# Performance work log

Hardware: AMD Instinct MI355X
Metric: run time of the kernel (lower is better)

## Reference

```python
import jax, jax.numpy as jnp
import numpy as np

B, C_IN, C_OUT = 16, 256, 128
V_RAW, N_VERT, K = 10242, 40962, 7


def setup_inputs() -> dict:
    key = jax.random.key(0)
    k1, k2, k3, k4, k5, k6 = jax.random.split(key, 6)
    x = jax.random.normal(k1, (B, C_IN, V_RAW), dtype=jnp.float32)
    W = jax.random.normal(k2, (C_OUT, C_IN), dtype=jnp.float32) * (1.0 / np.sqrt(C_IN))
    b = jax.random.normal(k3, (C_OUT,), dtype=jnp.float32) * 0.01
    up_neigh_indices = jax.random.randint(k4, (N_VERT, K), 0, N_VERT, dtype=jnp.int64)
    down_indices = jax.random.randint(k5, (V_RAW,), 0, N_VERT, dtype=jnp.int64)
    max_pool_indices = jax.random.randint(k6, (B, C_OUT, V_RAW), 0, K, dtype=jnp.int64)
    return {"x": x, "W": W, "b": b,
            "up_neigh_indices": up_neigh_indices,
            "down_indices": down_indices,
            "max_pool_indices": max_pool_indices}


def _feats_indices(n_feats: int, n_raw_vertices: int) -> np.ndarray:
    # torch: floor(linspace(0, n_feats, num=n_raw_vertices*n_feats)); last -= 1
    fi = np.floor(np.linspace(0.0, float(n_feats), num=n_raw_vertices * n_feats))
    fi[-1] -= 1
    return fi.astype(np.int64)


def reference(x, W, b, up_neigh_indices, down_indices, max_pool_indices):
    n_samples, in_feats, n_raw = x.shape
    n_vertices = up_neigh_indices.shape[0]
    out_feats = W.shape[0]

    # per-vertex linear projection: (B, Cin, V) -> (B, Cout, V)
    h = jnp.einsum('bcv,oc->bov', x, W) + b[None, :, None]

    # neighbor table at coarse vertices: (V_raw, K)
    neigh = up_neigh_indices[down_indices]

    # vertices_indices[b, f, v] = neigh[v, max_pool_indices[b, f, v]]
    vi = neigh[jnp.arange(n_raw)[None, None, :], max_pool_indices]  # (B, Cout, V_raw)

    # flatten exactly like torch (row-major over (Cout, V_raw))
    h_flat = h.reshape(n_samples, out_feats * n_raw)
    vi_flat = vi.reshape(n_samples, out_feats * n_raw)
    fi = jnp.asarray(_feats_indices(out_feats, n_raw))  # (Cout*V_raw,) static

    y = jnp.zeros((n_samples, out_feats, n_vertices), dtype=h.dtype)
    y = y.at[jnp.arange(n_samples)[:, None], fi[None, :], vi_flat].set(h_flat)
    return y
```

## Files before the change

kernel.cpp:

```cpp
#include <hip/hip_runtime.h>

#define NB    16
#define CIN   256
#define COUT  128
#define VRAW  10242
#define NVERT 40962
#define QSZ   10241
#define NROW  (NB * COUT)

typedef __attribute__((ext_vector_type(8))) short short8;
typedef __attribute__((ext_vector_type(4))) float floatx4;
typedef float f4u __attribute__((ext_vector_type(4), aligned(4)));

__device__ inline unsigned short f2bf(float f) {
    unsigned u = __builtin_bit_cast(unsigned, f);
    u += 0x7fffu + ((u >> 16) & 1u);
    return (unsigned short)(u >> 16);
}

__global__ __launch_bounds__(256) void convw_kernel(const float* __restrict__ W,
                                                    unsigned short* __restrict__ Wbf) {
    int i = blockIdx.x * 256 + threadIdx.x;
    Wbf[i] = f2bf(W[i]);
}

__global__ __launch_bounds__(256) void prep_kernel(const int* __restrict__ up,
                                                   const int* __restrict__ down,
                                                   unsigned short* __restrict__ T16) {
    int idx = blockIdx.x * 256 + threadIdx.x;
    if (idx >= VRAW * 8) return;
    int v = idx >> 3;
    int k = idx & 7;
    if (k > 6) k = 6;
    T16[idx] = (unsigned short)up[down[v] * 7 + k];
}

__global__ __launch_bounds__(256) void tgt_kernel(const int* __restrict__ mpi,
                                                  const unsigned short* __restrict__ T16,
                                                  unsigned* __restrict__ tgt32) {
    const int r  = blockIdx.y;
    const int vp = blockIdx.x * 256 + threadIdx.x;
    if (vp >= VRAW / 2) return;
    const int2 kk = *(const int2*)(mpi + (size_t)r * VRAW + 2 * (size_t)vp);
    const unsigned t0 = T16[(2 * vp)     * 8 + kk.x];
    const unsigned t1 = T16[(2 * vp + 1) * 8 + kk.y];
    tgt32[(size_t)r * (VRAW / 2) + vp] = t0 | (t1 << 16);
}

#define KC 64
#define VT 128
__global__ __launch_bounds__(256) void gemm_kernel(const float* __restrict__ x,
                                                   const unsigned short* __restrict__ Wbf,
                                                   const float* __restrict__ bias,
                                                   float* __restrict__ h) {
    __shared__ unsigned short xt[VT * KC];
    const int b    = blockIdx.y;
    const int v0   = blockIdx.x * VT;
    const int tid  = threadIdx.x;
    const int wv   = tid >> 6;
    const int lane = tid & 63;
    const int mn   = lane & 15;
    const int q    = lane >> 4;
    const int ow   = (wv & 1) * 64;
    const int vwl  = (wv >> 1) * 64;

    floatx4 acc[4][4];
#pragma unroll
    for (int ot = 0; ot < 4; ot++)
#pragma unroll
        for (int vt = 0; vt < 4; vt++) acc[ot][vt] = (floatx4)0.f;

    for (int c0 = 0; c0 < CIN; c0 += KC) {
#pragma unroll
        for (int i = 0; i < 2; i++) {
            const int tile  = tid + i * 256;
            const int cg    = tile >> 5;
            const int vg    = tile & 31;
            const int vglob = v0 + vg * 4;
            const float* xp = x + ((size_t)b * CIN + c0 + cg * 4) * VRAW + vglob;
            float vals[4][4];
            if (vglob + 3 < VRAW) {
#pragma unroll
                for (int cc = 0; cc < 4; cc++) {
                    f4u rv = *(const f4u*)(xp + (size_t)cc * VRAW);
                    vals[cc][0] = rv.x; vals[cc][1] = rv.y;
                    vals[cc][2] = rv.z; vals[cc][3] = rv.w;
                }
            } else {
#pragma unroll
                for (int cc = 0; cc < 4; cc++)
#pragma unroll
                    for (int jj = 0; jj < 4; jj++)
                        vals[cc][jj] = (vglob + jj < VRAW) ? xp[(size_t)cc * VRAW + jj] : 0.f;
            }
            const int swbase = (cg ^ ((vg & 7) << 1)) << 2;
#pragma unroll
            for (int jj = 0; jj < 4; jj++) {
                const int vloc = vg * 4 + jj;
                unsigned long long pk =
                      (unsigned long long)f2bf(vals[0][jj])
                    | ((unsigned long long)f2bf(vals[1][jj]) << 16)
                    | ((unsigned long long)f2bf(vals[2][jj]) << 32)
                    | ((unsigned long long)f2bf(vals[3][jj]) << 48);
                *(unsigned long long*)&xt[vloc * KC + swbase] = pk;
            }
        }
        __syncthreads();

#pragma unroll
        for (int kk = 0; kk < 2; kk++) {
            short8 bfrag[4];
#pragma unroll
            for (int vt = 0; vt < 4; vt++) {
                const int vloc = vwl + vt * 16 + mn;
                const int cqb  = kk * 8 + q * 2;
                const int cq   = cqb ^ (((vloc >> 2) & 7) << 1);
                bfrag[vt] = *(const short8*)&xt[vloc * KC + (cq << 2)];
            }
#pragma unroll
            for (int ot = 0; ot < 4; ot++) {
                const short8 afrag = *(const short8*)(Wbf + (size_t)(ow + ot * 16 + mn) * CIN
                                                      + c0 + kk * 32 + q * 8);
#pragma unroll
                for (int vt = 0; vt < 4; vt++)
                    acc[ot][vt] = __builtin_amdgcn_mfma_f32_16x16x32_bf16(afrag, bfrag[vt], acc[ot][vt], 0, 0, 0);
            }
        }
        __syncthreads();
    }

#pragma unroll
    for (int ot = 0; ot < 4; ot++) {
#pragma unroll
        for (int r = 0; r < 4; r++) {
            const int o  = ow + ot * 16 + q * 4 + r;
            const float bi = bias[o];
#pragma unroll
            for (int vt = 0; vt < 4; vt++) {
                const int v = v0 + vwl + vt * 16 + mn;
                if (v < VRAW) h[((size_t)b * COUT + o) * VRAW + v] = acc[ot][vt][r] + bi;
            }
        }
    }
}

template<int USE_TGT>
__global__ __launch_bounds__(512, 6) void scatter_kernel(const unsigned* __restrict__ tgt32,
                                                         const unsigned short* __restrict__ T16,
                                                         const int* __restrict__ mpi,
                                                         const float* __restrict__ h,
                                                         float* __restrict__ y) {
    __shared__ __align__(16) unsigned st[QSZ];
    const int bid = blockIdx.x;
    const int x8  = bid & 7;
    const int j   = bid >> 3;
    const int r   = x8 * 256 + (j >> 2);
    const int qi  = j & 3;
    const int tbase = qi * QSZ;
    const int qlen  = min(QSZ, NVERT - tbase);
    const int tid   = threadIdx.x;

    uint4* st4 = (uint4*)st;
    const uint4 z4 = make_uint4(0u, 0u, 0u, 0u);
#pragma unroll
    for (int i = 0; i < 5; i++) st4[tid + i * 512] = z4;
    if (tid == 0) st[10240] = 0u;
    __syncthreads();

    if (USE_TGT) {
        const unsigned* tRow = tgt32 + (size_t)r * (VRAW / 2);
#pragma unroll
        for (int it = 0; it < 10; it++) {
            const int vp = tid + it * 512;
            const unsigned tw = tRow[vp];
            const unsigned lt0 = (tw & 0xffffu) - (unsigned)tbase;
            const unsigned lt1 = (tw >> 16)     - (unsigned)tbase;
            if (lt0 < (unsigned)qlen) atomicMax(&st[lt0], (unsigned)(2 * vp + 1));
            if (lt1 < (unsigned)qlen) atomicMax(&st[lt1], (unsigned)(2 * vp + 2));
        }
        if (tid == 0) {
            const unsigned tw = tRow[5120];
            const unsigned lt0 = (tw & 0xffffu) - (unsigned)tbase;
            const unsigned lt1 = (tw >> 16)     - (unsigned)tbase;
            if (lt0 < (unsigned)qlen) atomicMax(&st[lt0], 10241u);
            if (lt1 < (unsigned)qlen) atomicMax(&st[lt1], 10242u);
        }
    } else {
        const int* mpiRow = mpi + (size_t)r * VRAW;
#pragma unroll 4
        for (int it = 0; it < 20; it++) {
            const int v = tid + it * 512;
            const int k = mpiRow[v];
            const uint4 tt = *(const uint4*)(T16 + (size_t)v * 8);
            const unsigned w0 = (k & 2) ? tt.y : tt.x;
            const unsigned w1 = (k & 2) ? tt.w : tt.z;
            const unsigned wsel = (k & 4) ? w1 : w0;
            const unsigned t = (wsel >> ((k & 1) * 16)) & 0xffffu;
            const unsigned lt = t - (unsigned)tbase;
            if (lt < (unsigned)qlen) atomicMax(&st[lt], (unsigned)(v + 1));
        }
        if (tid < 2) {
            const int v = 10240 + tid;
            const int k = mpiRow[v];
            const uint4 tt = *(const uint4*)(T16 + (size_t)v * 8);
            const unsigned w0 = (k & 2) ? tt.y : tt.x;
            const unsigned w1 = (k & 2) ? tt.w : tt.z;
            const unsigned wsel = (k & 4) ? w1 : w0;
            const unsigned t = (wsel >> ((k & 1) * 16)) & 0xffffu;
            const unsigned lt = t - (unsigned)tbase;
            if (lt < (unsigned)qlen) atomicMax(&st[lt], (unsigned)(v + 1));
        }
    }
    __syncthreads();

    const float* hRow = h + (size_t)r * VRAW;
    float* yRow = y + (size_t)r * NVERT + tbase;
#pragma unroll
    for (int i2 = 0; i2 < 4; i2++) {
        const int i = tid + i2 * 512;
        const uint4 s4 = st4[i];
        f4u out;
        out.x = s4.x ? hRow[s4.x - 1u] : 0.f;
        out.y = s4.y ? hRow[s4.y - 1u] : 0.f;
        out.z = s4.z ? hRow[s4.z - 1u] : 0.f;
        out.w = s4.w ? hRow[s4.w - 1u] : 0.f;
        *(f4u*)(yRow + 4 * i) = out;
    }
    {
        const int i = tid + 2048;
        if (4 * i + 3 < qlen) {
            const uint4 s4 = st4[i];
            f4u out;
            out.x = s4.x ? hRow[s4.x - 1u] : 0.f;
            out.y = s4.y ? hRow[s4.y - 1u] : 0.f;
            out.z = s4.z ? hRow[s4.z - 1u] : 0.f;
            out.w = s4.w ? hRow[s4.w - 1u] : 0.f;
            *(f4u*)(yRow + 4 * i) = out;
        }
    }
    const int base = qlen & ~3;
    if (tid < qlen - base) {
        const int lt = base + tid;
        const unsigned s = st[lt];
        yRow[lt] = s ? hRow[s - 1u] : 0.f;
    }
}

extern "C" void kernel_launch(void* const* d_in, const int* in_sizes, int n_in,
                              void* d_out, int out_size, void* d_ws, size_t ws_size,
                              hipStream_t stream) {
    const float* x    = (const float*)d_in[0];
    const float* W    = (const float*)d_in[1];
    const float* bias = (const float*)d_in[2];
    const int*   up   = (const int*)d_in[3];
    const int*   down = (const int*)d_in[4];
    const int*   mpi  = (const int*)d_in[5];
    float* y = (float*)d_out;

    const size_t off_h   = 65536;
    const size_t off_t16 = off_h + (size_t)NROW * VRAW * 4;
    const size_t off_tgt = off_t16 + (size_t)VRAW * 8 * 2;
    const size_t need    = off_tgt + (size_t)NROW * (VRAW / 2) * 4;

    unsigned short* Wbf = (unsigned short*)d_ws;
    float* h            = (float*)((char*)d_ws + off_h);
    unsigned short* T16 = (unsigned short*)((char*)d_ws + off_t16);
    unsigned* tgt32     = (unsigned*)((char*)d_ws + off_tgt);
    const bool use_tgt  = ws_size >= need;

    convw_kernel<<<COUT * CIN / 256, 256, 0, stream>>>(W, Wbf);
    prep_kernel<<<(VRAW * 8 + 255) / 256, 256, 0, stream>>>(up, down, T16);
    if (use_tgt) {
        dim3 tgrid((VRAW / 2 + 255) / 256, NROW);
        tgt_kernel<<<tgrid, 256, 0, stream>>>(mpi, T16, tgt32);
    }

    dim3 ggrid((VRAW + VT - 1) / VT, NB);
    gemm_kernel<<<ggrid, 256, 0, stream>>>(x, Wbf, bias, h);

    if (use_tgt)
        scatter_kernel<1><<<NROW * 4, 512, 0, stream>>>(tgt32, T16, mpi, h, y);
    else
        scatter_kernel<0><<<NROW * 4, 512, 0, stream>>>(tgt32, T16, mpi, h, y);
}
```

Baseline: 690.7 us.

## Double-buffer GEMM input tile in LDS with register prefetch of next K chunk

The GEMM kernel now keeps two LDS buffers for the bf16 x tile. It issues the global loads for the next 64-channel chunk into registers before running the MFMAs on the current chunk, then converts and writes them into the other buffer afterwards. This removes one barrier per iteration and is meant to hide global load latency behind matrix math. In exchange it doubles LDS use (32KB) and holds the 32 prefetched floats per thread in registers, which may lower occupancy.

```diff
diff --git a/kernel.cpp b/kernel.cpp
--- a/kernel.cpp
+++ b/kernel.cpp
@@ -49,11 +49,12 @@
 
 #define KC 64
 #define VT 128
+
 __global__ __launch_bounds__(256) void gemm_kernel(const float* __restrict__ x,
                                                    const unsigned short* __restrict__ Wbf,
                                                    const float* __restrict__ bias,
                                                    float* __restrict__ h) {
-    __shared__ unsigned short xt[VT * KC];
+    __shared__ unsigned short xt[2][VT * KC];
     const int b    = blockIdx.y;
     const int v0   = blockIdx.x * VT;
     const int tid  = threadIdx.x;
@@ -70,43 +71,62 @@
 #pragma unroll
         for (int vt = 0; vt < 4; vt++) acc[ot][vt] = (floatx4)0.f;
 
-    for (int c0 = 0; c0 < CIN; c0 += KC) {
-#pragma unroll
-        for (int i = 0; i < 2; i++) {
-            const int tile  = tid + i * 256;
-            const int cg    = tile >> 5;
-            const int vg    = tile & 31;
-            const int vglob = v0 + vg * 4;
-            const float* xp = x + ((size_t)b * CIN + c0 + cg * 4) * VRAW + vglob;
-            float vals[4][4];
-            if (vglob + 3 < VRAW) {
-#pragma unroll
-                for (int cc = 0; cc < 4; cc++) {
-                    f4u rv = *(const f4u*)(xp + (size_t)cc * VRAW);
-                    vals[cc][0] = rv.x; vals[cc][1] = rv.y;
-                    vals[cc][2] = rv.z; vals[cc][3] = rv.w;
-                }
-            } else {
-#pragma unroll
-                for (int cc = 0; cc < 4; cc++)
-#pragma unroll
-                    for (int jj = 0; jj < 4; jj++)
-                        vals[cc][jj] = (vglob + jj < VRAW) ? xp[(size_t)cc * VRAW + jj] : 0.f;
-            }
-            const int swbase = (cg ^ ((vg & 7) << 1)) << 2;
-#pragma unroll
-            for (int jj = 0; jj < 4; jj++) {
-                const int vloc = vg * 4 + jj;
-                unsigned long long pk =
-                      (unsigned long long)f2bf(vals[0][jj])
-                    | ((unsigned long long)f2bf(vals[1][jj]) << 16)
-                    | ((unsigned long long)f2bf(vals[2][jj]) << 32)
-                    | ((unsigned long long)f2bf(vals[3][jj]) << 48);
-                *(unsigned long long*)&xt[vloc * KC + swbase] = pk;
-            }
-        }
+    float vals[2][4][4];
+
+#define LOADX(c0_)                                                                  \
+    {                                                                               \
+        _Pragma("unroll")                                                           \
+        for (int i = 0; i < 2; i++) {                                               \
+            const int cg    = (tid >> 5) + i * 8;                                   \
+            const int vg    = tid & 31;                                             \
+            const int vglob = v0 + vg * 4;                                          \
+            const float* xp = x + ((size_t)b * CIN + (c0_) + cg * 4) * VRAW + vglob;\
+            if (vglob + 3 < VRAW) {                                                 \
+                _Pragma("unroll")                                                   \
+                for (int cc = 0; cc < 4; cc++) {                                    \
+                    f4u rv = *(const f4u*)(xp + (size_t)cc * VRAW);                 \
+                    vals[i][cc][0] = rv.x; vals[i][cc][1] = rv.y;                   \
+                    vals[i][cc][2] = rv.z; vals[i][cc][3] = rv.w;                   \
+                }                                                                   \
+            } else {                                                                \
+                _Pragma("unroll")                                                   \
+                for (int cc = 0; cc < 4; cc++)                                      \
+                    _Pragma("unroll")                                               \
+                    for (int jj = 0; jj < 4; jj++)                                  \
+                        vals[i][cc][jj] = (vglob + jj < VRAW) ? xp[(size_t)cc * VRAW + jj] : 0.f; \
+            }                                                                       \
+        }                                                                           \
+    }
+
+#define CWRITE(buf_)                                                                \
+    {                                                                               \
+        _Pragma("unroll")                                                           \
+        for (int i = 0; i < 2; i++) {                                               \
+            const int cg     = (tid >> 5) + i * 8;                                  \
+            const int vg     = tid & 31;                                            \
+            const int swbase = (cg ^ ((vg & 7) << 1)) << 2;                         \
+            _Pragma("unroll")                                                       \
+            for (int jj = 0; jj < 4; jj++) {                                        \
+                const int vloc = vg * 4 + jj;                                       \
+                unsigned long long pk =                                             \
+                      (unsigned long long)f2bf(vals[i][0][jj])                      \
+                    | ((unsigned long long)f2bf(vals[i][1][jj]) << 16)              \
+                    | ((unsigned long long)f2bf(vals[i][2][jj]) << 32)              \
+                    | ((unsigned long long)f2bf(vals[i][3][jj]) << 48);             \
+                *(unsigned long long*)&(buf_)[vloc * KC + swbase] = pk;             \
+            }                                                                       \
+        }                                                                           \
+    }
+
+    LOADX(0);
+    CWRITE(xt[0]);
+
+    for (int ck = 0; ck < 4; ck++) {
+        const int c0 = ck * KC;
+        if (ck < 3) LOADX(c0 + KC);
         __syncthreads();
 
+        const unsigned short* buf = xt[ck & 1];
 #pragma unroll
         for (int kk = 0; kk < 2; kk++) {
             short8 bfrag[4];
@@ -115,7 +135,7 @@
                 const int vloc = vwl + vt * 16 + mn;
                 const int cqb  = kk * 8 + q * 2;
                 const int cq   = cqb ^ (((vloc >> 2) & 7) << 1);
-                bfrag[vt] = *(const short8*)&xt[vloc * KC + (cq << 2)];
+                bfrag[vt] = *(const short8*)&buf[vloc * KC + (cq << 2)];
             }
 #pragma unroll
             for (int ot = 0; ot < 4; ot++) {
@@ -126,19 +146,22 @@
                     acc[ot][vt] = __builtin_amdgcn_mfma_f32_16x16x32_bf16(afrag, bfrag[vt], acc[ot][vt], 0, 0, 0);
             }
         }
-        __syncthreads();
-    }
+
+        if (ck < 3) CWRITE(xt[(ck + 1) & 1]);
+    }
+#undef LOADX
+#undef CWRITE
 
 #pragma unroll
     for (int ot = 0; ot < 4; ot++) {
 #pragma unroll
-        for (int r = 0; r < 4; r++) {
-            const int o  = ow + ot * 16 + q * 4 + r;
+        for (int rr = 0; rr < 4; rr++) {
+            const int o  = ow + ot * 16 + q * 4 + rr;
             const float bi = bias[o];
 #pragma unroll
             for (int vt = 0; vt < 4; vt++) {
                 const int v = v0 + vwl + vt * 16 + mn;
-                if (v < VRAW) h[((size_t)b * COUT + o) * VRAW + v] = acc[ot][vt][r] + bi;
+                if (v < VRAW) h[((size_t)b * COUT + o) * VRAW + v] = acc[ot][vt][rr] + bi;
             }
         }
     }
```

Result: no change. 699.0 us (+1.2%).
